# Performance work log

Hardware: AMD Instinct MI355X
Metric: run time of the kernel (lower is better)

The kernel has to match this reference:

```python
import jax, jax.numpy as jnp
import numpy as np

NUM_EMB = 1024
EMB_DIM = 32


def setup_inputs() -> dict:
    key = jax.random.key(0)
    k1, k2 = jax.random.split(key)
    z = jax.random.normal(k1, (32, EMB_DIM, 64, 64), dtype=jnp.float32)
    # nn.Embedding weight init: uniform(-1/num_embeddings, 1/num_embeddings)
    emb_weight = jax.random.uniform(
        k2, (NUM_EMB, EMB_DIM), dtype=jnp.float32,
        minval=-1.0 / NUM_EMB, maxval=1.0 / NUM_EMB)
    return {"z": z, "emb_weight": emb_weight}


def reference(z, emb_weight):
    # z: [B, C, H, W] -> [B, H, W, C]
    z_p = jnp.transpose(z, (0, 2, 3, 1))
    B, H, W, C = z_p.shape
    z_flat = z_p.reshape(-1, C)  # [N, C]
    # squared distances via expansion: ||z||^2 + ||e||^2 - 2 z.e  -> [N, K]
    d = (jnp.sum(z_flat * z_flat, axis=1, keepdims=True)
         + jnp.sum(emb_weight * emb_weight, axis=1)
         - 2.0 * jnp.matmul(z_flat, emb_weight.T))
    idx = jnp.argmin(d, axis=1)  # [N]
    z_q = emb_weight[idx].reshape(B, H, W, C)
    # straight-through estimator (applied in BHWC, then back to BCHW)
    z_q = z_p + jax.lax.stop_gradient(z_q - z_p)
    z_q = jnp.transpose(z_q, (0, 3, 1, 2))  # [B, C, H, W]
    return z_q, idx
```

## Files before the change

kernel.cpp:

```cpp
#include <hip/hip_runtime.h>


#define NUM_EMB 1024
#define EMB_DIM 32
#define HW      4096
#define BATCH   32
#define N_TOT   (BATCH * HW)
#define NSPLIT  4
#define CODES_PER (NUM_EMB / NSPLIT)
#define MARGIN  1.0e-4f
#define CHUNK   256

#define OFF_BQ    0u
#define OFF_EH    4096u
#define OFF_CTRS  135168u
#define OFF_LISTB 135184u
#define WS_NEED   659472u
#define WS_NEED_R7 (4096u + 4u * 131072u * 8u)

using f16x8 = __attribute__((ext_vector_type(8))) _Float16;
using f32x4 = __attribute__((ext_vector_type(4))) float;

#define REPEAT32(M) \
    M(0)  M(1)  M(2)  M(3)  M(4)  M(5)  M(6)  M(7)  \
    M(8)  M(9)  M(10) M(11) M(12) M(13) M(14) M(15) \
    M(16) M(17) M(18) M(19) M(20) M(21) M(22) M(23) \
    M(24) M(25) M(26) M(27) M(28) M(29) M(30) M(31)

__device__ __forceinline__ float pairwise_sq32(const float* __restrict__ e) {
    float r0 = __fmul_rn(e[0], e[0]), r1 = __fmul_rn(e[1], e[1]);
    float r2 = __fmul_rn(e[2], e[2]), r3 = __fmul_rn(e[3], e[3]);
    float r4 = __fmul_rn(e[4], e[4]), r5 = __fmul_rn(e[5], e[5]);
    float r6 = __fmul_rn(e[6], e[6]), r7 = __fmul_rn(e[7], e[7]);
#pragma unroll
    for (int i = 8; i < 32; i += 8) {
        r0 = __fadd_rn(r0, __fmul_rn(e[i + 0], e[i + 0]));
        r1 = __fadd_rn(r1, __fmul_rn(e[i + 1], e[i + 1]));
        r2 = __fadd_rn(r2, __fmul_rn(e[i + 2], e[i + 2]));
        r3 = __fadd_rn(r3, __fmul_rn(e[i + 3], e[i + 3]));
        r4 = __fadd_rn(r4, __fmul_rn(e[i + 4], e[i + 4]));
        r5 = __fadd_rn(r5, __fmul_rn(e[i + 5], e[i + 5]));
        r6 = __fadd_rn(r6, __fmul_rn(e[i + 6], e[i + 6]));
        r7 = __fadd_rn(r7, __fmul_rn(e[i + 7], e[i + 7]));
    }
    return __fadd_rn(__fadd_rn(__fadd_rn(r0, r1), __fadd_rn(r2, r3)),
                     __fadd_rn(__fadd_rn(r4, r5), __fadd_rn(r6, r7)));
}

__device__ __forceinline__ void store_row16(unsigned short* dst,
                                            const unsigned short* v) {
    unsigned w[16];
#pragma unroll
    for (int i = 0; i < 16; ++i)
        w[i] = (unsigned)v[2 * i] | ((unsigned)v[2 * i + 1] << 16);
    uint4* d4 = (uint4*)dst;
    d4[0] = make_uint4(w[0], w[1], w[2], w[3]);
    d4[1] = make_uint4(w[4], w[5], w[6], w[7]);
    d4[2] = make_uint4(w[8], w[9], w[10], w[11]);
    d4[3] = make_uint4(w[12], w[13], w[14], w[15]);
}

__global__ __launch_bounds__(256) void vq_prep_e(
        const float* __restrict__ emb, float* __restrict__ bq,
        unsigned short* __restrict__ eh, int* __restrict__ ctrs) {
    const int g = blockIdx.x * 256 + threadIdx.x;
    if (g < 2) ctrs[g] = 0;
    if (g >= NUM_EMB) return;
    const float* e = emb + g * EMB_DIM;
    bq[g] = pairwise_sq32(e);
    unsigned short h[32];
#pragma unroll
    for (int c = 0; c < 32; ++c) {
        _Float16 hv = (_Float16)(-2.0f * e[c]);
        h[c] = __builtin_bit_cast(unsigned short, hv);
    }
    store_row16(eh + (size_t)g * 32, h);
}

#define LOADZ(c) float z##c = zp[(size_t)(c) * HW];
#define Z_SQ_A()                                                              \
    float r0 = __fmul_rn(z0, z0), r1 = __fmul_rn(z1, z1);                     \
    float r2 = __fmul_rn(z2, z2), r3 = __fmul_rn(z3, z3);                     \
    float r4 = __fmul_rn(z4, z4), r5 = __fmul_rn(z5, z5);                     \
    float r6 = __fmul_rn(z6, z6), r7 = __fmul_rn(z7, z7);                     \
    r0 = __fadd_rn(r0, __fmul_rn(z8,  z8));  r0 = __fadd_rn(r0, __fmul_rn(z16, z16)); \
    r0 = __fadd_rn(r0, __fmul_rn(z24, z24));                                  \
    r1 = __fadd_rn(r1, __fmul_rn(z9,  z9));  r1 = __fadd_rn(r1, __fmul_rn(z17, z17)); \
    r1 = __fadd_rn(r1, __fmul_rn(z25, z25));                                  \
    r2 = __fadd_rn(r2, __fmul_rn(z10, z10)); r2 = __fadd_rn(r2, __fmul_rn(z18, z18)); \
    r2 = __fadd_rn(r2, __fmul_rn(z26, z26));                                  \
    r3 = __fadd_rn(r3, __fmul_rn(z11, z11)); r3 = __fadd_rn(r3, __fmul_rn(z19, z19)); \
    r3 = __fadd_rn(r3, __fmul_rn(z27, z27));                                  \
    r4 = __fadd_rn(r4, __fmul_rn(z12, z12)); r4 = __fadd_rn(r4, __fmul_rn(z20, z20)); \
    r4 = __fadd_rn(r4, __fmul_rn(z28, z28));                                  \
    r5 = __fadd_rn(r5, __fmul_rn(z13, z13)); r5 = __fadd_rn(r5, __fmul_rn(z21, z21)); \
    r5 = __fadd_rn(r5, __fmul_rn(z29, z29));                                  \
    r6 = __fadd_rn(r6, __fmul_rn(z14, z14)); r6 = __fadd_rn(r6, __fmul_rn(z22, z22)); \
    r6 = __fadd_rn(r6, __fmul_rn(z30, z30));                                  \
    r7 = __fadd_rn(r7, __fmul_rn(z15, z15)); r7 = __fadd_rn(r7, __fmul_rn(z23, z23)); \
    r7 = __fadd_rn(r7, __fmul_rn(z31, z31));                                  \
    const float a = __fadd_rn(                                                \
        __fadd_rn(__fadd_rn(r0, r1), __fadd_rn(r2, r3)),                      \
        __fadd_rn(__fadd_rn(r4, r5), __fadd_rn(r6, r7)));

#define FMA1(k) m = __fmaf_rn(z##k, e[(k)], m);
#define EXACT_KEY(jv)                                                         \
    {                                                                         \
        const float* e = emb + (size_t)(jv) * EMB_DIM;                        \
        float m = 0.0f;                                                       \
        REPEAT32(FMA1)                                                        \
        float d = __fsub_rn(__fadd_rn(a, bq[(jv)]), __fmul_rn(2.0f, m));      \
        unsigned u = __float_as_uint(d);                                      \
        u = (u & 0x80000000u) ? ~u : (u | 0x80000000u);                       \
        unsigned long long kk =                                               \
            ((unsigned long long)u << 32) | (unsigned)(jv);                   \
        if (kk < bestk) bestk = kk;                                           \
    }

__global__ __launch_bounds__(256, 8) void vq_filter(
        const float* __restrict__ z, const float* __restrict__ emb,
        const unsigned short* __restrict__ eh,
        const float* __restrict__ bq, int* __restrict__ ctrs,
        int* __restrict__ listB, float* __restrict__ out_zq,
        float* __restrict__ out_idx) {
    __shared__ __align__(16) char smem[19968];
    _Float16* seh = (_Float16*)smem;
    float*    sbq = (float*)(smem + 16384);
    float* sz    = (float*)smem;
    int*   scand = (int*)(smem + 16896);
    int*   sdest = (int*)(smem + 18944);
    int*   sidx  = (int*)(smem + 19456);
    __shared__ int swt[2];
    __shared__ int sbase1;

    const int tid  = threadIdx.x;
    const int lane = tid & 63;
    const int wv   = tid >> 6;
    const int cloc = lane & 15, quad = lane >> 4;
    const int qbase = blockIdx.x * 128 + wv * 32;

    float zf[2][8];
    f16x8 az[2];
#pragma unroll
    for (int t = 0; t < 2; ++t) {
        const int q  = qbase + t * 16 + cloc;
        const int b  = q >> 12;
        const int hw = q & 4095;
        const float* zb = z + ((size_t)b * EMB_DIM + quad * 8) * HW + hw;
#pragma unroll
        for (int k = 0; k < 8; ++k) {
            float v = zb[(size_t)k * HW];
            zf[t][k] = v;
            az[t][k] = (_Float16)v;
        }
    }

    float m1[2][4], m2[2][4];
    int   i1[2][4];
#pragma unroll
    for (int t = 0; t < 2; ++t)
#pragma unroll
        for (int r = 0; r < 4; ++r) {
            m1[t][r] = 3.4e38f; m2[t][r] = 3.4e38f; i1[t][r] = 0;
        }

    for (int ch = 0; ch < 4; ++ch) {
        if (ch) __syncthreads();
        {
            const uint4* src = (const uint4*)(eh + (size_t)ch * CHUNK * 32);
            uint4* dst = (uint4*)seh;
#pragma unroll
            for (int i = 0; i < 4; ++i) dst[i * 256 + tid] = src[i * 256 + tid];
            sbq[tid] = bq[ch * CHUNK + tid];
        }
        __syncthreads();

        for (int jt = 0; jt < 16; ++jt) {
            const int row = jt * 16 + cloc;
            f16x8 ef = *(const f16x8*)(seh + row * 32 + quad * 8);
            const float bqv = sbq[row];
            const int jts = ch * 16 + jt;
#pragma unroll
            for (int t = 0; t < 2; ++t) {
                f32x4 acc = {bqv, bqv, bqv, bqv};
                acc = __builtin_amdgcn_mfma_f32_16x16x32_f16(az[t], ef, acc, 0, 0, 0);
#pragma unroll
                for (int r = 0; r < 4; ++r) {
                    const float tt = acc[r];
                    const bool l1 = tt < m1[t][r];
                    m2[t][r] = __builtin_amdgcn_fmed3f(tt, m1[t][r], m2[t][r]);
                    m1[t][r] = fminf(m1[t][r], tt);
                    i1[t][r] = l1 ? jts : i1[t][r];
                }
            }
        }
    }
    __syncthreads();

#pragma unroll
    for (int t = 0; t < 2; ++t) {
        const int ql = wv * 32 + t * 16 + cloc;
#pragma unroll
        for (int k = 0; k < 8; ++k) sz[ql * 33 + quad * 8 + k] = zf[t][k];
    }

    float g[2][4];
#pragma unroll
    for (int t = 0; t < 2; ++t)
#pragma unroll
        for (int r = 0; r < 4; ++r) g[t][r] = m1[t][r];
#pragma unroll
    for (int off = 1; off < 16; off <<= 1)
#pragma unroll
        for (int t = 0; t < 2; ++t)
#pragma unroll
            for (int r = 0; r < 4; ++r)
                g[t][r] = fminf(g[t][r], __shfl_xor(g[t][r], off, 64));

#pragma unroll
    for (int t = 0; t < 2; ++t)
#pragma unroll
        for (int r = 0; r < 4; ++r) {
            const float thr = g[t][r] + MARGIN;
            const int   ql  = wv * 32 + t * 16 + quad * 4 + r;
            const bool  f1  = m1[t][r] <= thr;
            const bool  f2  = m2[t][r] <= thr;
            const unsigned long long b1 = __ballot(f1);
            const unsigned long long b2 = __ballot(f2);
            const unsigned mk1 = (unsigned)(b1 >> (quad * 16)) & 0xFFFFu;
            const unsigned mk2 = (unsigned)(b2 >> (quad * 16)) & 0xFFFFu;
            const int pc  = __popc(mk1);
            const int ldr = __ffs(mk1) - 1;
            if (mk2 | (unsigned)(pc > 4)) {
                if (cloc == ldr) sdest[ql] = 5;
            } else {
                if (f1)
                    scand[(ql << 2) + __popc(mk1 & ((1u << cloc) - 1u))] =
                        i1[t][r] * 16 + cloc;
                if (cloc == ldr) sdest[ql] = pc;
            }
        }
    __syncthreads();

    int d = 0, pre = 0;
    if (tid < 128) {
        d = sdest[tid];
        const unsigned long long mB = __ballot(d == 5);
        pre = (int)__popcll(mB & ((1ull << lane) - 1ull));
        if (lane == 0) swt[tid >> 6] = (int)__popcll(mB);
    }
    __syncthreads();
    if (tid == 0) {
        const int tB = swt[0] + swt[1];
        sbase1 = tB ? atomicAdd(&ctrs[1], tB) : 0;
    }
    __syncthreads();
    if (tid < 128) {
        if (d == 5) {
            listB[sbase1 + ((tid >> 6) ? swt[0] : 0) + pre] =
                blockIdx.x * 128 + tid;
        } else if (d == 1) {
            sidx[tid] = scand[tid << 2];
        } else {
            const float* szp = &sz[tid * 33];
#define LOADZ2(c) const float z##c = szp[(c)];
            REPEAT32(LOADZ2)
#undef LOADZ2
            Z_SQ_A()
            unsigned long long bestk = ~0ull;
            for (int k = 0; k < d; ++k) {
                const int jv = scand[(tid << 2) + k];
                EXACT_KEY(jv)
            }
            sidx[tid] = (int)(unsigned)(bestk & 0xffffffffu);
        }
    }
    __syncthreads();

    if (tid < 128 && d != 5) {
        const int n    = blockIdx.x * 128 + tid;
        const int bidx = sidx[tid];
        out_idx[n] = (float)bidx;
        const int b  = n >> 12;
        const int hw = n & 4095;
        const float4* er = (const float4*)(emb + (size_t)bidx * EMB_DIM);
        float* op = out_zq + (size_t)b * EMB_DIM * HW + hw;
#pragma unroll
        for (int c4 = 0; c4 < 8; ++c4) {
            float4 v = er[c4];
            op[(size_t)(c4 * 4 + 0) * HW] = v.x;
            op[(size_t)(c4 * 4 + 1) * HW] = v.y;
            op[(size_t)(c4 * 4 + 2) * HW] = v.z;
            op[(size_t)(c4 * 4 + 3) * HW] = v.w;
        }
    }
}

__global__ __launch_bounds__(256) void vq_fixup(
        const float* __restrict__ z, const float* __restrict__ emb,
        const float* __restrict__ bq, const int* __restrict__ ctrs,
        const int* __restrict__ listB, float* __restrict__ out_zq,
        float* __restrict__ out_idx) {
    __shared__ unsigned long long bs[256];
    const int tid = threadIdx.x;
    const int total = ctrs[1];

    for (int it = blockIdx.x; it < total; it += gridDim.x) {
        const int n  = listB[it];
        const int b  = n >> 12;
        const int hw = n & 4095;
        const float* zp = z + (size_t)b * EMB_DIM * HW + hw;
        REPEAT32(LOADZ)
        Z_SQ_A()
        unsigned long long bestk = ~0ull;
#pragma unroll
        for (int k = 0; k < 4; ++k) { const int jv = tid * 4 + k; EXACT_KEY(jv) }
        bs[tid] = bestk;
        __syncthreads();
        for (int off = 128; off > 0; off >>= 1) {
            if (tid < off && bs[tid + off] < bs[tid]) bs[tid] = bs[tid + off];
            __syncthreads();
        }
        const int bidx = (int)(unsigned)(bs[0] & 0xffffffffu);
        if (tid == 0) out_idx[n] = (float)bidx;
        if (tid < EMB_DIM)
            out_zq[(size_t)b * EMB_DIM * HW + (size_t)tid * HW + hw] =
                emb[(size_t)bidx * EMB_DIM + tid];
        __syncthreads();
    }
}

#define SCAN_GROUP4(j)                                                        \
    {                                                                         \
        const float* e = emb + (size_t)(j) * EMB_DIM;                         \
        const float bq0 = bq[(j) + 0], bq1 = bq[(j) + 1];                     \
        const float bq2 = bq[(j) + 2], bq3 = bq[(j) + 3];                     \
        float m0 = 0.0f, m1 = 0.0f, m2 = 0.0f, m3 = 0.0f;                     \
        REPEAT32(FMA_K)                                                       \
        float d0 = __fsub_rn(__fadd_rn(a, bq0), __fmul_rn(2.0f, m0));         \
        float d1 = __fsub_rn(__fadd_rn(a, bq1), __fmul_rn(2.0f, m1));         \
        float d2 = __fsub_rn(__fadd_rn(a, bq2), __fmul_rn(2.0f, m2));         \
        float d3 = __fsub_rn(__fadd_rn(a, bq3), __fmul_rn(2.0f, m3));         \
        if (d0 < best) { best = d0; bidx = (j) + 0; }                         \
        if (d1 < best) { best = d1; bidx = (j) + 1; }                         \
        if (d2 < best) { best = d2; bidx = (j) + 2; }                         \
        if (d3 < best) { best = d3; bidx = (j) + 3; }                         \
    }
#define FMA_K(k) \
        m0 = __fmaf_rn(z##k, e[0 * EMB_DIM + (k)], m0); \
        m1 = __fmaf_rn(z##k, e[1 * EMB_DIM + (k)], m1); \
        m2 = __fmaf_rn(z##k, e[2 * EMB_DIM + (k)], m2); \
        m3 = __fmaf_rn(z##k, e[3 * EMB_DIM + (k)], m3);

__global__ __launch_bounds__(256) void vq_sqnorm_kernel(
        const float* __restrict__ emb, float* __restrict__ bq) {
    int j = blockIdx.x * 256 + threadIdx.x;
    if (j < NUM_EMB) bq[j] = pairwise_sq32(emb + j * EMB_DIM);
}

__global__ __launch_bounds__(128, 4) void vq_partial_kernel(
        const float* __restrict__ z, const float* __restrict__ emb,
        const float* __restrict__ bq, unsigned long long* __restrict__ pk) {
    const int n  = blockIdx.x * 128 + threadIdx.x;
    const int b  = n >> 12;
    const int hw = n & 4095;
    const float* zp = z + (size_t)b * EMB_DIM * HW + hw;
    REPEAT32(LOADZ)
    Z_SQ_A()
    const int j0 = blockIdx.y * CODES_PER;
    float best = 3.4e38f;
    int   bidx = j0;
    for (int j = j0; j < j0 + CODES_PER; j += 4) SCAN_GROUP4(j)
    pk[(size_t)blockIdx.y * N_TOT + n] =
        ((unsigned long long)__float_as_uint(best) << 32) | (unsigned)bidx;
}

__global__ __launch_bounds__(256, 2) void vq_main_kernel(
        const float* __restrict__ z, const float* __restrict__ emb,
        const float* __restrict__ bq, float* __restrict__ out_zq,
        float* __restrict__ out_idx) {
    const int n  = blockIdx.x * 256 + threadIdx.x;
    const int b  = n >> 12;
    const int hw = n & 4095;
    const float* zp = z + (size_t)b * EMB_DIM * HW + hw;
    REPEAT32(LOADZ)
    Z_SQ_A()
    float best = 3.4e38f;
    int   bidx = 0;
    for (int j = 0; j < NUM_EMB; j += 4) SCAN_GROUP4(j)
    out_idx[n] = (float)bidx;
    const float* eb = emb + (size_t)bidx * EMB_DIM;
    float* op = out_zq + (size_t)b * EMB_DIM * HW + hw;
#pragma unroll
    for (int cc = 0; cc < EMB_DIM; ++cc) op[(size_t)cc * HW] = eb[cc];
}

__global__ __launch_bounds__(256) void vq_combine_kernel(
        const float* __restrict__ emb,
        const unsigned long long* __restrict__ pk,
        float* __restrict__ out_zq, float* __restrict__ out_idx) {
    const int n = blockIdx.x * 256 + threadIdx.x;
    unsigned long long m = pk[n];
#pragma unroll
    for (int y = 1; y < NSPLIT; ++y) {
        unsigned long long v = pk[(size_t)y * N_TOT + n];
        if (v < m) m = v;
    }
    const int bidx = (int)(unsigned)(m & 0xffffffffu);
    out_idx[n] = (float)bidx;
    const int b  = n >> 12;
    const int hw = n & 4095;
    const float* eb = emb + (size_t)bidx * EMB_DIM;
    float* op = out_zq + (size_t)b * EMB_DIM * HW + hw;
#pragma unroll
    for (int cc = 0; cc < EMB_DIM; ++cc) op[(size_t)cc * HW] = eb[cc];
}

extern "C" void kernel_launch(void* const* d_in, const int* in_sizes, int n_in,
                              void* d_out, int out_size, void* d_ws,
                              size_t ws_size, hipStream_t stream) {
    const float* z   = (const float*)d_in[0];
    const float* emb = (const float*)d_in[1];
    char* ws = (char*)d_ws;
    float* out0 = (float*)d_out;
    float* out1 = out0 + (size_t)BATCH * EMB_DIM * HW;

    if (ws_size >= WS_NEED) {
        float*          bq    = (float*)(ws + OFF_BQ);
        unsigned short* eh    = (unsigned short*)(ws + OFF_EH);
        int*            ctrs  = (int*)(ws + OFF_CTRS);
        int*            listB = (int*)(ws + OFF_LISTB);

        vq_prep_e<<<4, 256, 0, stream>>>(emb, bq, eh, ctrs);
        vq_filter<<<N_TOT / 128, 256, 0, stream>>>(z, emb, eh, bq, ctrs,
                                                   listB, out0, out1);
        vq_fixup<<<1024, 256, 0, stream>>>(z, emb, bq, ctrs, listB,
                                           out0, out1);
    } else if (ws_size >= WS_NEED_R7) {
        float* bq = (float*)ws;
        unsigned long long* pk = (unsigned long long*)(ws + 4096);
        vq_sqnorm_kernel<<<NUM_EMB / 256, 256, 0, stream>>>(emb, bq);
        vq_partial_kernel<<<dim3(N_TOT / 128, NSPLIT), 128, 0, stream>>>(
            z, emb, bq, pk);
        vq_combine_kernel<<<N_TOT / 256, 256, 0, stream>>>(emb, pk, out0, out1);
    } else {
        float* bq = (float*)ws;
        vq_sqnorm_kernel<<<NUM_EMB / 256, 256, 0, stream>>>(emb, bq);
        vq_main_kernel<<<N_TOT / 256, 256, 0, stream>>>(z, emb, bq, out0, out1);
    }
}
```

Before: 147.0 us.

## Fuse fixup into filter kernel and pack code index into distance bits

Removes the separate fixup kernel and its global atomic list: each filter block now handles its own ambiguous points in-block, reducing the fp32 exact rescan to a block-wide reduction per point. The top-2 tracking packs the tile index into the low mantissa bits of the fp16-MFMA distance, dropping the separate index register and its select. The z values are no longer held in registers or staged through shared memory; the exact path reloads them from global. Launch bounds occupancy hint drops from 8 to 4, and blocks with many ambiguous points now serialize that work inside the block.

After: 131.7 us. -10.4%, faster.

```diff
diff --git a/kernel.cpp b/kernel.cpp
--- a/kernel.cpp
+++ b/kernel.cpp
@@ -13,9 +13,7 @@
 
 #define OFF_BQ    0u
 #define OFF_EH    4096u
-#define OFF_CTRS  135168u
-#define OFF_LISTB 135184u
-#define WS_NEED   659472u
+#define WS_NEED   69632u
 #define WS_NEED_R7 (4096u + 4u * 131072u * 8u)
 
 using f16x8 = __attribute__((ext_vector_type(8))) _Float16;
@@ -62,9 +60,8 @@
 
 __global__ __launch_bounds__(256) void vq_prep_e(
         const float* __restrict__ emb, float* __restrict__ bq,
-        unsigned short* __restrict__ eh, int* __restrict__ ctrs) {
+        unsigned short* __restrict__ eh) {
     const int g = blockIdx.x * 256 + threadIdx.x;
-    if (g < 2) ctrs[g] = 0;
     if (g >= NUM_EMB) return;
     const float* e = emb + g * EMB_DIM;
     bq[g] = pairwise_sq32(e);
@@ -117,21 +114,20 @@
         if (kk < bestk) bestk = kk;                                           \
     }
 
-__global__ __launch_bounds__(256, 8) void vq_filter(
+__global__ __launch_bounds__(256, 4) void vq_filter(
         const float* __restrict__ z, const float* __restrict__ emb,
         const unsigned short* __restrict__ eh,
-        const float* __restrict__ bq, int* __restrict__ ctrs,
-        int* __restrict__ listB, float* __restrict__ out_zq,
-        float* __restrict__ out_idx) {
-    __shared__ __align__(16) char smem[19968];
+        const float* __restrict__ bq,
+        float* __restrict__ out_zq, float* __restrict__ out_idx) {
+    __shared__ __align__(16) char smem[17408];
     _Float16* seh = (_Float16*)smem;
     float*    sbq = (float*)(smem + 16384);
-    float* sz    = (float*)smem;
-    int*   scand = (int*)(smem + 16896);
-    int*   sdest = (int*)(smem + 18944);
-    int*   sidx  = (int*)(smem + 19456);
+    int* scand  = (int*)smem;
+    int* sdest  = (int*)(smem + 2048);
+    int* sBlist = (int*)(smem + 2560);
+    unsigned long long* bs =
+        (unsigned long long*)(smem + 3072);
     __shared__ int swt[2];
-    __shared__ int sbase1;
 
     const int tid  = threadIdx.x;
     const int lane = tid & 63;
@@ -139,7 +135,6 @@
     const int cloc = lane & 15, quad = lane >> 4;
     const int qbase = blockIdx.x * 128 + wv * 32;
 
-    float zf[2][8];
     f16x8 az[2];
 #pragma unroll
     for (int t = 0; t < 2; ++t) {
@@ -148,21 +143,17 @@
         const int hw = q & 4095;
         const float* zb = z + ((size_t)b * EMB_DIM + quad * 8) * HW + hw;
 #pragma unroll
-        for (int k = 0; k < 8; ++k) {
-            float v = zb[(size_t)k * HW];
-            zf[t][k] = v;
-            az[t][k] = (_Float16)v;
-        }
+        for (int k = 0; k < 8; ++k)
+            az[t][k] = (_Float16)zb[(size_t)k * HW];
     }
 
     float m1[2][4], m2[2][4];
-    int   i1[2][4];
 #pragma unroll
     for (int t = 0; t < 2; ++t)
 #pragma unroll
-        for (int r = 0; r < 4; ++r) {
-            m1[t][r] = 3.4e38f; m2[t][r] = 3.4e38f; i1[t][r] = 0;
-        }
+        for (int r = 0; r < 4; ++r) { m1[t][r] = 3.4e38f; m2[t][r] = 3.4e38f; }
+
+    const unsigned km = 0xFFFFFFC0u;
 
     for (int ch = 0; ch < 4; ++ch) {
         if (ch) __syncthreads();
@@ -175,34 +166,43 @@
         }
         __syncthreads();
 
+        float c1[2][4], c2[2][4];
+#pragma unroll
+        for (int t = 0; t < 2; ++t)
+#pragma unroll
+            for (int r = 0; r < 4; ++r) { c1[t][r] = 3.4e38f; c2[t][r] = 3.4e38f; }
+
+#pragma unroll
         for (int jt = 0; jt < 16; ++jt) {
             const int row = jt * 16 + cloc;
             f16x8 ef = *(const f16x8*)(seh + row * 32 + quad * 8);
             const float bqv = sbq[row];
-            const int jts = ch * 16 + jt;
 #pragma unroll
             for (int t = 0; t < 2; ++t) {
                 f32x4 acc = {bqv, bqv, bqv, bqv};
                 acc = __builtin_amdgcn_mfma_f32_16x16x32_f16(az[t], ef, acc, 0, 0, 0);
 #pragma unroll
                 for (int r = 0; r < 4; ++r) {
-                    const float tt = acc[r];
-                    const bool l1 = tt < m1[t][r];
-                    m2[t][r] = __builtin_amdgcn_fmed3f(tt, m1[t][r], m2[t][r]);
-                    m1[t][r] = fminf(m1[t][r], tt);
-                    i1[t][r] = l1 ? jts : i1[t][r];
+                    const float kv = __uint_as_float(
+                        (__float_as_uint(acc[r]) & km) | (unsigned)jt);
+                    c2[t][r] = __builtin_amdgcn_fmed3f(kv, c1[t][r], c2[t][r]);
+                    c1[t][r] = fminf(c1[t][r], kv);
                 }
             }
         }
+
+        const unsigned chb = (unsigned)ch << 4;
+#pragma unroll
+        for (int t = 0; t < 2; ++t)
+#pragma unroll
+            for (int r = 0; r < 4; ++r) {
+                const float a1 = __uint_as_float(__float_as_uint(c1[t][r]) | chb);
+                const float a2 = __uint_as_float(__float_as_uint(c2[t][r]) | chb);
+                m2[t][r] = fminf(fmaxf(m1[t][r], a1), fminf(m2[t][r], a2));
+                m1[t][r] = fminf(m1[t][r], a1);
+            }
     }
     __syncthreads();
-
-#pragma unroll
-    for (int t = 0; t < 2; ++t) {
-        const int ql = wv * 32 + t * 16 + cloc;
-#pragma unroll
-        for (int k = 0; k < 8; ++k) sz[ql * 33 + quad * 8 + k] = zf[t][k];
-    }
 
     float g[2][4];
 #pragma unroll
@@ -236,7 +236,7 @@
             } else {
                 if (f1)
                     scand[(ql << 2) + __popc(mk1 & ((1u << cloc) - 1u))] =
-                        i1[t][r] * 16 + cloc;
+                        (int)(__float_as_uint(m1[t][r]) & 63u) * 16 + cloc;
                 if (cloc == ldr) sdest[ql] = pc;
             }
         }
@@ -250,41 +250,36 @@
         if (lane == 0) swt[tid >> 6] = (int)__popcll(mB);
     }
     __syncthreads();
-    if (tid == 0) {
-        const int tB = swt[0] + swt[1];
-        sbase1 = tB ? atomicAdd(&ctrs[1], tB) : 0;
-    }
-    __syncthreads();
+    int myidx = 0;
     if (tid < 128) {
         if (d == 5) {
-            listB[sbase1 + ((tid >> 6) ? swt[0] : 0) + pre] =
-                blockIdx.x * 128 + tid;
+            sBlist[((tid >> 6) ? swt[0] : 0) + pre] = tid;
         } else if (d == 1) {
-            sidx[tid] = scand[tid << 2];
+            myidx = scand[tid << 2];
         } else {
-            const float* szp = &sz[tid * 33];
-#define LOADZ2(c) const float z##c = szp[(c)];
-            REPEAT32(LOADZ2)
-#undef LOADZ2
+            const int n  = blockIdx.x * 128 + tid;
+            const int bb = n >> 12;
+            const int hh = n & 4095;
+            const float* zp = z + (size_t)bb * EMB_DIM * HW + hh;
+            REPEAT32(LOADZ)
             Z_SQ_A()
             unsigned long long bestk = ~0ull;
             for (int k = 0; k < d; ++k) {
                 const int jv = scand[(tid << 2) + k];
                 EXACT_KEY(jv)
             }
-            sidx[tid] = (int)(unsigned)(bestk & 0xffffffffu);
+            myidx = (int)(unsigned)(bestk & 0xffffffffu);
         }
     }
     __syncthreads();
 
     if (tid < 128 && d != 5) {
         const int n    = blockIdx.x * 128 + tid;
-        const int bidx = sidx[tid];
-        out_idx[n] = (float)bidx;
-        const int b  = n >> 12;
-        const int hw = n & 4095;
-        const float4* er = (const float4*)(emb + (size_t)bidx * EMB_DIM);
-        float* op = out_zq + (size_t)b * EMB_DIM * HW + hw;
+        out_idx[n] = (float)myidx;
+        const int bb = n >> 12;
+        const int hh = n & 4095;
+        const float4* er = (const float4*)(emb + (size_t)myidx * EMB_DIM);
+        float* op = out_zq + (size_t)bb * EMB_DIM * HW + hh;
 #pragma unroll
         for (int c4 = 0; c4 < 8; ++c4) {
             float4 v = er[c4];
@@ -294,22 +289,14 @@
             op[(size_t)(c4 * 4 + 3) * HW] = v.w;
         }
     }
-}
-
-__global__ __launch_bounds__(256) void vq_fixup(
-        const float* __restrict__ z, const float* __restrict__ emb,
-        const float* __restrict__ bq, const int* __restrict__ ctrs,
-        const int* __restrict__ listB, float* __restrict__ out_zq,
-        float* __restrict__ out_idx) {
-    __shared__ unsigned long long bs[256];
-    const int tid = threadIdx.x;
-    const int total = ctrs[1];
-
-    for (int it = blockIdx.x; it < total; it += gridDim.x) {
-        const int n  = listB[it];
-        const int b  = n >> 12;
-        const int hw = n & 4095;
-        const float* zp = z + (size_t)b * EMB_DIM * HW + hw;
+
+    const int nB = swt[0] + swt[1];
+    for (int ib = 0; ib < nB; ++ib) {
+        const int ql = sBlist[ib];
+        const int n  = blockIdx.x * 128 + ql;
+        const int bb = n >> 12;
+        const int hh = n & 4095;
+        const float* zp = z + (size_t)bb * EMB_DIM * HW + hh;
         REPEAT32(LOADZ)
         Z_SQ_A()
         unsigned long long bestk = ~0ull;
@@ -321,11 +308,11 @@
             if (tid < off && bs[tid + off] < bs[tid]) bs[tid] = bs[tid + off];
             __syncthreads();
         }
-        const int bidx = (int)(unsigned)(bs[0] & 0xffffffffu);
-        if (tid == 0) out_idx[n] = (float)bidx;
+        const int fb = (int)(unsigned)(bs[0] & 0xffffffffu);
+        if (tid == 0) out_idx[n] = (float)fb;
         if (tid < EMB_DIM)
-            out_zq[(size_t)b * EMB_DIM * HW + (size_t)tid * HW + hw] =
-                emb[(size_t)bidx * EMB_DIM + tid];
+            out_zq[(size_t)bb * EMB_DIM * HW + (size_t)tid * HW + hh] =
+                emb[(size_t)fb * EMB_DIM + tid];
         __syncthreads();
     }
 }
@@ -426,16 +413,12 @@
     float* out1 = out0 + (size_t)BATCH * EMB_DIM * HW;
 
     if (ws_size >= WS_NEED) {
-        float*          bq    = (float*)(ws + OFF_BQ);
-        unsigned short* eh    = (unsigned short*)(ws + OFF_EH);
-        int*            ctrs  = (int*)(ws + OFF_CTRS);
-        int*            listB = (int*)(ws + OFF_LISTB);
-
-        vq_prep_e<<<4, 256, 0, stream>>>(emb, bq, eh, ctrs);
-        vq_filter<<<N_TOT / 128, 256, 0, stream>>>(z, emb, eh, bq, ctrs,
-                                                   listB, out0, out1);
-        vq_fixup<<<1024, 256, 0, stream>>>(z, emb, bq, ctrs, listB,
-                                           out0, out1);
+        float*          bq = (float*)(ws + OFF_BQ);
+        unsigned short* eh = (unsigned short*)(ws + OFF_EH);
+
+        vq_prep_e<<<4, 256, 0, stream>>>(emb, bq, eh);
+        vq_filter<<<N_TOT / 128, 256, 0, stream>>>(z, emb, eh, bq,
+                                                   out0, out1);
     } else if (ws_size >= WS_NEED_R7) {
         float* bq = (float*)ws;
         unsigned long long* pk = (unsigned long long*)(ws + 4096);
```
